# Kernel tuning notes

Hardware: AMD Instinct MI355X
Metric: run time of the kernel (lower is better)

The kernel has to match this reference:

```python
import jax, jax.numpy as jnp
import numpy as np

IMG = 640.0  # nominal image size for box coordinates
EPS_IOU = 1e-9   # eps used by iou_calculator
EPS_OVL = 1e-6   # eps used by bbox_overlaps


def _make_boxes(key, lead_shape):
    # Build valid <x1,y1,x2,y2> boxes: random centers in [0, IMG), sizes in [4, 204).
    k1, k2 = jax.random.split(key)
    c = jax.random.uniform(k1, lead_shape + (2,), dtype=jnp.float32) * IMG
    wh = jax.random.uniform(k2, lead_shape + (2,), dtype=jnp.float32) * 200.0 + 4.0
    return jnp.concatenate([c - wh / 2.0, c + wh / 2.0], axis=-1)


def setup_inputs() -> dict:
    key = jax.random.key(0)
    ka, kb, kc = jax.random.split(key, 3)
    gt_bboxes = _make_boxes(ka, (16, 128))        # (bs, n_max_boxes, 4)
    pred_bboxes = _make_boxes(kb, (16, 8400))     # (bs, num_total_anchors, 4)
    anchor_bboxes = _make_boxes(kc, (8400,))      # (num_total_anchors, 4)
    return {"gt_bboxes": gt_bboxes, "pred_bboxes": pred_bboxes, "anchor_bboxes": anchor_bboxes}


def _dist_calculator(gt_flat, anchor_bboxes):
    # gt_flat: (bs*M, 4), anchor_bboxes: (N, 4) -> distances (bs*M, N), ac_points (N, 2)
    gt_pts = (gt_flat[:, :2] + gt_flat[:, 2:]) / 2.0
    ac_pts = (anchor_bboxes[:, :2] + anchor_bboxes[:, 2:]) / 2.0
    d = jnp.sqrt(jnp.sum((gt_pts[:, None, :] - ac_pts[None, :, :]) ** 2, axis=-1))
    return d, ac_pts


def _iou_calculator(box1, box2, eps=EPS_IOU):
    # box1: (bs, M, 4), box2: (bs, N, 4) -> (bs, M, N) pairwise IoU
    b1 = box1[:, :, None, :]
    b2 = box2[:, None, :, :]
    lt = jnp.maximum(b1[..., :2], b2[..., :2])
    rb = jnp.minimum(b1[..., 2:], b2[..., 2:])
    wh = jnp.clip(rb - lt, 0.0)
    overlap = wh[..., 0] * wh[..., 1]
    area1 = (b1[..., 2] - b1[..., 0]) * (b1[..., 3] - b1[..., 1])
    area2 = (b2[..., 2] - b2[..., 0]) * (b2[..., 3] - b2[..., 1])
    union = area1 + area2 - overlap + eps
    return overlap / union


def _bbox_overlaps_giou(b1, b2, eps=EPS_OVL):
    # b1: (M, 4), b2: (N, 4) -> (M, N) pairwise GIoU (bbox_overlaps, mode='giou', is_aligned=False)
    area1 = (b1[:, 2] - b1[:, 0]) * (b1[:, 3] - b1[:, 1])
    area2 = (b2[:, 2] - b2[:, 0]) * (b2[:, 3] - b2[:, 1])
    lt = jnp.maximum(b1[:, None, :2], b2[None, :, :2])
    rb = jnp.minimum(b1[:, None, 2:], b2[None, :, 2:])
    wh = jnp.clip(rb - lt, 0.0)
    overlap = wh[..., 0] * wh[..., 1]
    union = jnp.maximum(area1[:, None] + area2[None, :] - overlap, eps)
    ious = overlap / union
    enclosed_lt = jnp.minimum(b1[:, None, :2], b2[None, :, :2])
    enclosed_rb = jnp.maximum(b1[:, None, 2:], b2[None, :, 2:])
    enclose_wh = jnp.clip(enclosed_rb - enclosed_lt, 0.0)
    enclose_area = jnp.maximum(enclose_wh[..., 0] * enclose_wh[..., 1], eps)
    return ious - (enclose_area - union) / enclose_area


def reference(gt_bboxes, pred_bboxes, anchor_bboxes):
    bs, M, _ = gt_bboxes.shape
    gt_flat = gt_bboxes.reshape(bs * M, 4)
    # ATSS assigner stage: center distance gt<->anchor and gt<->anchor GIoU
    distances, ac_points = _dist_calculator(gt_flat, anchor_bboxes)
    gious = _bbox_overlaps_giou(gt_flat, anchor_bboxes)
    # TAL assigner stage: batched pairwise IoU gt<->pred
    overlaps = _iou_calculator(gt_bboxes, pred_bboxes)
    return distances, overlaps, gious
```

## Files before the change

kernel.cpp:

```cpp
#include <hip/hip_runtime.h>


#define EPS_IOU 1e-9f
#define EPS_OVL 1e-6f
#define ROWS 4

typedef float vfloat4 __attribute__((ext_vector_type(4)));

__device__ __forceinline__ float frcp(float x)  { return __builtin_amdgcn_rcpf(x); }
__device__ __forceinline__ float fsqrtf_(float x){ return __builtin_amdgcn_sqrtf(x); }

__device__ __forceinline__ void nt_store4(float* p, float a, float b, float c, float d) {
    vfloat4 v; v.x = a; v.y = b; v.z = c; v.w = d;
    __builtin_nontemporal_store(v, (vfloat4*)p);
}

__global__ __launch_bounds__(256) void yolov6_fused(
    const float4* __restrict__ gt,
    const float4* __restrict__ pred,
    const float4* __restrict__ anc,
    float* __restrict__ out_dist,
    float* __restrict__ out_ovl,
    float* __restrict__ out_giou,
    int N, int M, int qcols, int total)
{
    const int t = blockIdx.x * blockDim.x + threadIdx.x;
    if (t >= total) return;

    const int rb = t / qcols;
    const int c  = t - rb * qcols;
    const int j  = c * 4;
    if (j >= N) return;
    const int g0 = rb * ROWS;
    const int b  = g0 / M;

    float4 ab[4], pb[4];
    float acx[4], acy[4], aarea[4], parea[4];
    const float4* ancp  = anc + j;
    const float4* predp = pred + (long long)b * N + j;
#pragma unroll
    for (int k = 0; k < 4; ++k) {
        ab[k] = ancp[k];
        pb[k] = predp[k];
        acx[k]   = (ab[k].x + ab[k].z) * 0.5f;
        acy[k]   = (ab[k].y + ab[k].w) * 0.5f;
        aarea[k] = (ab[k].z - ab[k].x) * (ab[k].w - ab[k].y);
        parea[k] = (pb[k].z - pb[k].x) * (pb[k].w - pb[k].y);
    }

#pragma unroll
    for (int r = 0; r < ROWS; ++r) {
        const int g = g0 + r;
        const float4 gb = gt[g];
        const float gcx   = (gb.x + gb.z) * 0.5f;
        const float gcy   = (gb.y + gb.w) * 0.5f;
        const float garea = (gb.z - gb.x) * (gb.w - gb.y);

        float dv[4], ov[4], gv[4];
#pragma unroll
        for (int k = 0; k < 4; ++k) {
            float dx = gcx - acx[k], dy = gcy - acy[k];
            dv[k] = fsqrtf_(dx * dx + dy * dy);
            {
                float ltx = fmaxf(gb.x, ab[k].x), lty = fmaxf(gb.y, ab[k].y);
                float rbx = fminf(gb.z, ab[k].z), rby = fminf(gb.w, ab[k].w);
                float w = fmaxf(rbx - ltx, 0.0f), h = fmaxf(rby - lty, 0.0f);
                float overlap = w * h;
                float uni = fmaxf(garea + aarea[k] - overlap, EPS_OVL);
                float elx = fminf(gb.x, ab[k].x), ely = fminf(gb.y, ab[k].y);
                float erx = fmaxf(gb.z, ab[k].z), ery = fmaxf(gb.w, ab[k].w);
                float ew = fmaxf(erx - elx, 0.0f), eh = fmaxf(ery - ely, 0.0f);
                float earea = fmaxf(ew * eh, EPS_OVL);
                float num = overlap * earea - (earea - uni) * uni;
                gv[k] = num * frcp(uni * earea);
            }
            {
                float ltx = fmaxf(gb.x, pb[k].x), lty = fmaxf(gb.y, pb[k].y);
                float rbx = fminf(gb.z, pb[k].z), rby = fminf(gb.w, pb[k].w);
                float w = fmaxf(rbx - ltx, 0.0f), h = fmaxf(rby - lty, 0.0f);
                float overlap = w * h;
                float uni = garea + parea[k] - overlap + EPS_IOU;
                ov[k] = overlap * frcp(uni);
            }
        }
        const long long row = (long long)g * N + j;
        nt_store4(out_dist + row, dv[0], dv[1], dv[2], dv[3]);
        nt_store4(out_ovl  + row, ov[0], ov[1], ov[2], ov[3]);
        nt_store4(out_giou + row, gv[0], gv[1], gv[2], gv[3]);
    }
}

extern "C" void kernel_launch(void* const* d_in, const int* in_sizes, int n_in,
                              void* d_out, int out_size, void* d_ws, size_t ws_size,
                              hipStream_t stream) {
    const float4* gt   = (const float4*)d_in[0];
    const float4* pred = (const float4*)d_in[1];
    const float4* anc  = (const float4*)d_in[2];

    const int N  = in_sizes[2] / 4;
    const int bs = in_sizes[1] / in_sizes[2];
    const int GM = in_sizes[0] / 4;
    const int M  = GM / bs;

    float* out = (float*)d_out;
    const long long plane = (long long)GM * N;
    float* out_dist = out;
    float* out_ovl  = out + plane;
    float* out_giou = out + 2 * plane;

    const int qcols = (N + 3) / 4;
    const int total = (GM / ROWS) * qcols;
    dim3 block(256);
    dim3 grid((total + 255) / 256);
    yolov6_fused<<<grid, block, 0, stream>>>(gt, pred, anc,
                                             out_dist, out_ovl, out_giou,
                                             N, M, qcols, total);
}
```

Baseline: 215.0 us.

## Split fused kernel into three per-output kernels with regular stores

Replaces the single fused kernel that wrote three output planes with three separate launches, one each for distance, IoU and GIoU. Each kernel writes one contiguous plane, and the stores become plain float4 stores instead of nontemporal ones. The aim is a simpler write stream per kernel with lower register pressure, at the cost of two extra launches and re-reading the anchor, gt and pred inputs.

```diff
diff --git a/kernel.cpp b/kernel.cpp
--- a/kernel.cpp
+++ b/kernel.cpp
@@ -5,28 +5,92 @@
 #define EPS_OVL 1e-6f
 #define ROWS 4
 
-typedef float vfloat4 __attribute__((ext_vector_type(4)));
-
-__device__ __forceinline__ float frcp(float x)  { return __builtin_amdgcn_rcpf(x); }
+__device__ __forceinline__ float frcp(float x)   { return __builtin_amdgcn_rcpf(x); }
 __device__ __forceinline__ float fsqrtf_(float x){ return __builtin_amdgcn_sqrtf(x); }
 
-__device__ __forceinline__ void nt_store4(float* p, float a, float b, float c, float d) {
-    vfloat4 v; v.x = a; v.y = b; v.z = c; v.w = d;
-    __builtin_nontemporal_store(v, (vfloat4*)p);
-}
-
-__global__ __launch_bounds__(256) void yolov6_fused(
-    const float4* __restrict__ gt,
-    const float4* __restrict__ pred,
-    const float4* __restrict__ anc,
-    float* __restrict__ out_dist,
-    float* __restrict__ out_ovl,
-    float* __restrict__ out_giou,
-    int N, int M, int qcols, int total)
+__global__ __launch_bounds__(256) void k_dist(
+    const float4* __restrict__ gt, const float4* __restrict__ anc,
+    float* __restrict__ out, int N, int qcols, int total)
 {
     const int t = blockIdx.x * blockDim.x + threadIdx.x;
     if (t >= total) return;
+    const int rb = t / qcols;
+    const int c  = t - rb * qcols;
+    const int j  = c * 4;
+    if (j >= N) return;
+    const int g0 = rb * ROWS;
 
+    float acx[4], acy[4];
+#pragma unroll
+    for (int k = 0; k < 4; ++k) {
+        float4 a = anc[j + k];
+        acx[k] = (a.x + a.z) * 0.5f;
+        acy[k] = (a.y + a.w) * 0.5f;
+    }
+#pragma unroll
+    for (int r = 0; r < ROWS; ++r) {
+        const float4 gb = gt[g0 + r];
+        const float gcx = (gb.x + gb.z) * 0.5f;
+        const float gcy = (gb.y + gb.w) * 0.5f;
+        float dv[4];
+#pragma unroll
+        for (int k = 0; k < 4; ++k) {
+            float dx = gcx - acx[k], dy = gcy - acy[k];
+            dv[k] = fsqrtf_(dx * dx + dy * dy);
+        }
+        *(float4*)(out + (long long)(g0 + r) * N + j) =
+            make_float4(dv[0], dv[1], dv[2], dv[3]);
+    }
+}
+
+__global__ __launch_bounds__(256) void k_giou(
+    const float4* __restrict__ gt, const float4* __restrict__ anc,
+    float* __restrict__ out, int N, int qcols, int total)
+{
+    const int t = blockIdx.x * blockDim.x + threadIdx.x;
+    if (t >= total) return;
+    const int rb = t / qcols;
+    const int c  = t - rb * qcols;
+    const int j  = c * 4;
+    if (j >= N) return;
+    const int g0 = rb * ROWS;
+
+    float4 ab[4]; float aarea[4];
+#pragma unroll
+    for (int k = 0; k < 4; ++k) {
+        ab[k] = anc[j + k];
+        aarea[k] = (ab[k].z - ab[k].x) * (ab[k].w - ab[k].y);
+    }
+#pragma unroll
+    for (int r = 0; r < ROWS; ++r) {
+        const float4 gb = gt[g0 + r];
+        const float garea = (gb.z - gb.x) * (gb.w - gb.y);
+        float gv[4];
+#pragma unroll
+        for (int k = 0; k < 4; ++k) {
+            float ltx = fmaxf(gb.x, ab[k].x), lty = fmaxf(gb.y, ab[k].y);
+            float rbx = fminf(gb.z, ab[k].z), rby = fminf(gb.w, ab[k].w);
+            float w = fmaxf(rbx - ltx, 0.0f), h = fmaxf(rby - lty, 0.0f);
+            float overlap = w * h;
+            float uni = fmaxf(garea + aarea[k] - overlap, EPS_OVL);
+            float elx = fminf(gb.x, ab[k].x), ely = fminf(gb.y, ab[k].y);
+            float erx = fmaxf(gb.z, ab[k].z), ery = fmaxf(gb.w, ab[k].w);
+            float ew = fmaxf(erx - elx, 0.0f), eh = fmaxf(ery - ely, 0.0f);
+            float earea = fmaxf(ew * eh, EPS_OVL);
+            float num = overlap * earea - (earea - uni) * uni;
+            gv[k] = num * frcp(uni * earea);
+        }
+        *(float4*)(out + (long long)(g0 + r) * N + j) =
+            make_float4(gv[0], gv[1], gv[2], gv[3]);
+    }
+}
+
+__global__ __launch_bounds__(256) void k_ovl(
+    const float4* __restrict__ gt, const float4* __restrict__ pred,
+    float* __restrict__ out, int N, int M, int qcols, int total)
+{
+    const int t = blockIdx.x * blockDim.x + threadIdx.x;
+    if (t >= total) return;
     const int rb = t / qcols;
     const int c  = t - rb * qcols;
     const int j  = c * 4;
@@ -34,59 +98,29 @@
     const int g0 = rb * ROWS;
     const int b  = g0 / M;
 
-    float4 ab[4], pb[4];
-    float acx[4], acy[4], aarea[4], parea[4];
-    const float4* ancp  = anc + j;
+    float4 pb[4]; float parea[4];
     const float4* predp = pred + (long long)b * N + j;
 #pragma unroll
     for (int k = 0; k < 4; ++k) {
-        ab[k] = ancp[k];
         pb[k] = predp[k];
-        acx[k]   = (ab[k].x + ab[k].z) * 0.5f;
-        acy[k]   = (ab[k].y + ab[k].w) * 0.5f;
-        aarea[k] = (ab[k].z - ab[k].x) * (ab[k].w - ab[k].y);
         parea[k] = (pb[k].z - pb[k].x) * (pb[k].w - pb[k].y);
     }
-
 #pragma unroll
     for (int r = 0; r < ROWS; ++r) {
-        const int g = g0 + r;
-        const float4 gb = gt[g];
-        const float gcx   = (gb.x + gb.z) * 0.5f;
-        const float gcy   = (gb.y + gb.w) * 0.5f;
+        const float4 gb = gt[g0 + r];
         const float garea = (gb.z - gb.x) * (gb.w - gb.y);
-
-        float dv[4], ov[4], gv[4];
+        float ov[4];
 #pragma unroll
         for (int k = 0; k < 4; ++k) {
-            float dx = gcx - acx[k], dy = gcy - acy[k];
-            dv[k] = fsqrtf_(dx * dx + dy * dy);
-            {
-                float ltx = fmaxf(gb.x, ab[k].x), lty = fmaxf(gb.y, ab[k].y);
-                float rbx = fminf(gb.z, ab[k].z), rby = fminf(gb.w, ab[k].w);
-                float w = fmaxf(rbx - ltx, 0.0f), h = fmaxf(rby - lty, 0.0f);
-                float overlap = w * h;
-                float uni = fmaxf(garea + aarea[k] - overlap, EPS_OVL);
-                float elx = fminf(gb.x, ab[k].x), ely = fminf(gb.y, ab[k].y);
-                float erx = fmaxf(gb.z, ab[k].z), ery = fmaxf(gb.w, ab[k].w);
-                float ew = fmaxf(erx - elx, 0.0f), eh = fmaxf(ery - ely, 0.0f);
-                float earea = fmaxf(ew * eh, EPS_OVL);
-                float num = overlap * earea - (earea - uni) * uni;
-                gv[k] = num * frcp(uni * earea);
-            }
-            {
-                float ltx = fmaxf(gb.x, pb[k].x), lty = fmaxf(gb.y, pb[k].y);
-                float rbx = fminf(gb.z, pb[k].z), rby = fminf(gb.w, pb[k].w);
-                float w = fmaxf(rbx - ltx, 0.0f), h = fmaxf(rby - lty, 0.0f);
-                float overlap = w * h;
-                float uni = garea + parea[k] - overlap + EPS_IOU;
-                ov[k] = overlap * frcp(uni);
-            }
+            float ltx = fmaxf(gb.x, pb[k].x), lty = fmaxf(gb.y, pb[k].y);
+            float rbx = fminf(gb.z, pb[k].z), rby = fminf(gb.w, pb[k].w);
+            float w = fmaxf(rbx - ltx, 0.0f), h = fmaxf(rby - lty, 0.0f);
+            float overlap = w * h;
+            float uni = garea + parea[k] - overlap + EPS_IOU;
+            ov[k] = overlap * frcp(uni);
         }
-        const long long row = (long long)g * N + j;
-        nt_store4(out_dist + row, dv[0], dv[1], dv[2], dv[3]);
-        nt_store4(out_ovl  + row, ov[0], ov[1], ov[2], ov[3]);
-        nt_store4(out_giou + row, gv[0], gv[1], gv[2], gv[3]);
+        *(float4*)(out + (long long)(g0 + r) * N + j) =
+            make_float4(ov[0], ov[1], ov[2], ov[3]);
     }
 }
 
@@ -112,7 +146,8 @@
     const int total = (GM / ROWS) * qcols;
     dim3 block(256);
     dim3 grid((total + 255) / 256);
-    yolov6_fused<<<grid, block, 0, stream>>>(gt, pred, anc,
-                                             out_dist, out_ovl, out_giou,
-                                             N, M, qcols, total);
+
+    k_dist<<<grid, block, 0, stream>>>(gt, anc,  out_dist, N, qcols, total);
+    k_ovl <<<grid, block, 0, stream>>>(gt, pred, out_ovl,  N, M, qcols, total);
+    k_giou<<<grid, block, 0, stream>>>(gt, anc,  out_giou, N, qcols, total);
 }
```

Result: slower. 222.1 us (+3.3%).
